# Optimization experiments

Measured on AMD Instinct MI355X. Metric: run time of the kernel, lower is better.

## Reference

```python
import jax, jax.numpy as jnp
import numpy as np

EPS = 1e-12  # torch F.normalize default eps


def setup_inputs() -> dict:
    key = jax.random.key(0)
    ks = jax.random.split(key, 7)
    dim, heads = 128, 8
    b, c, s, h, w = 2, dim, 3, 128, 128
    sc = 1.0 / np.sqrt(dim)
    return {
        "x": jax.random.normal(ks[0], (b, c, s, h, w), dtype=jnp.float32),
        "Wq": jax.random.normal(ks[1], (dim, dim), dtype=jnp.float32) * sc,
        "Wk": jax.random.normal(ks[2], (dim, dim), dtype=jnp.float32) * sc,
        "Wv": jax.random.normal(ks[3], (dim, dim), dtype=jnp.float32) * sc,
        "Wp": jax.random.normal(ks[4], (dim, dim), dtype=jnp.float32) * sc,
        "bp": jax.random.normal(ks[5], (dim,), dtype=jnp.float32) * 0.01,
        "rescale": jnp.ones((heads, 1, 1), dtype=jnp.float32),
    }


def _l2norm(t):
    # torch F.normalize(p=2, dim=-1): t / max(||t||, eps)
    n = jnp.sqrt(jnp.sum(t * t, axis=-1, keepdims=True))
    return t / jnp.maximum(n, EPS)


def reference(x, Wq, Wk, Wv, Wp, bp, rescale):
    b, c, s, h, w = x.shape
    heads = rescale.shape[0]
    d = c // heads
    n = h * w * s
    # [b,c,s,h,w] -> [b,h,w,s,c] -> [b, n, c]
    xt = jnp.transpose(x, (0, 3, 4, 2, 1)).reshape(b, n, c)
    # torch Linear: y = x @ W.T
    q = xt @ Wq.T
    k = xt @ Wk.T
    v = xt @ Wv.T
    # [b,n,heads,d] -> [b,heads,d,n] (channel attention: tokens along last axis)
    def to_heads(t):
        return jnp.transpose(t.reshape(b, n, heads, d), (0, 2, 3, 1))
    q, k, v = to_heads(q), to_heads(k), to_heads(v)
    q = _l2norm(q)
    k = _l2norm(k)
    # attn: [b,heads,d,d] = k @ q^T over token axis n
    attn = jnp.einsum('bhdn,bhen->bhde', k, q)
    attn = attn * rescale  # rescale broadcasts as [heads,1,1]
    attn = jax.nn.softmax(attn, axis=-1)
    out = jnp.einsum('bhde,bhen->bhdn', attn, v)  # [b,heads,d,n]
    # [b,heads,d,n] -> [b,n,heads*d]
    out = jnp.transpose(out, (0, 3, 1, 2)).reshape(b, n, c)
    out = out @ Wp.T + bp
    # [b,n,c] -> [b,h,w,s,c] -> [b,h,w,c,s] -> [b,c,s,h,w]
    out = out.reshape(b, h, w, s, c)
    out = jnp.transpose(out, (0, 1, 2, 4, 3))
    out = jnp.transpose(out, (0, 3, 4, 1, 2))
    return out
```

## Files before the change

### kernel.cpp

```cpp
#include <hip/hip_runtime.h>
#include <hip/hip_bf16.h>

typedef __bf16 bf16_t;
typedef __bf16 bf16x4 __attribute__((ext_vector_type(4)));
typedef __bf16 bf16x8 __attribute__((ext_vector_type(8)));
typedef float f32x4 __attribute__((ext_vector_type(4)));

#define NTOK 49152
#define CDIM 128
#define CHUNKS 128
#define KT 384
#define STEPS 12

__device__ inline f32x4 mfma16(bf16x8 a, bf16x8 b, f32x4 c) {
  return __builtin_amdgcn_mfma_f32_16x16x32_bf16(a, b, c, 0, 0, 0);
}

#define BARRIER() do { asm volatile("s_waitcnt lgkmcnt(0)" ::: "memory"); \
    __builtin_amdgcn_s_barrier(); } while (0)

#define STAGE_LOAD(st, step)                               \
  {                                                        \
    const float* p_ = gsrc + (step) * 32;                  \
    st[0] = *(const f32x4*)(p_ + 0);                       \
    st[1] = *(const f32x4*)(p_ + 4);                       \
    st[2] = *(const f32x4*)(p_ + 8);                       \
    st[3] = *(const f32x4*)(p_ + 12);                      \
  }
#define CVT4(v) (bf16x4){(bf16_t)(v)[0], (bf16_t)(v)[1], (bf16_t)(v)[2], (bf16_t)(v)[3]}
#define STAGE_WRITE(st, buf)                               \
  {                                                        \
    bf16_t* t_ = &tile[buf][0];                            \
    *(bf16x4*)&t_[cg0 * 8 + 0] = CVT4(st[0]);              \
    *(bf16x4*)&t_[cg0 * 8 + 4] = CVT4(st[1]);              \
    *(bf16x4*)&t_[cg1 * 8 + 0] = CVT4(st[2]);              \
    *(bf16x4*)&t_[cg1 * 8 + 4] = CVT4(st[3]);              \
  }
#define MFMA_PHASE(buf)                                                     \
  {                                                                         \
    bf16x8 frag[8];                                                         \
    _Pragma("unroll")                                                       \
    for (int g = 0; g < 8; ++g)                                             \
      frag[g] = *(const bf16x8*)&tile[buf][(g * 64 + lane) * 8];            \
    bf16x8 a0, a1;                                                          \
    if (wave == 0)      { a0 = frag[0]; a1 = frag[1]; }                     \
    else if (wave == 1) { a0 = frag[2]; a1 = frag[3]; }                     \
    else if (wave == 2) { a0 = frag[4]; a1 = frag[5]; }                     \
    else                { a0 = frag[6]; a1 = frag[7]; }                     \
    _Pragma("unroll")                                                       \
    for (int j = 0; j < 8; ++j) {                                           \
      acc[0][j] = mfma16(a0, frag[j], acc[0][j]);                           \
      acc[1][j] = mfma16(a1, frag[j], acc[1][j]);                           \
    }                                                                       \
  }

__global__ __launch_bounds__(256) void k1_gram(const float* __restrict__ x,
                                               float* __restrict__ part) {
  const int blk = blockIdx.x;
  const int b = blk >> 7, chunk = blk & 127;
  const float* Xb = x + (size_t)b * CDIM * NTOK;
  const int tid = threadIdx.x, wave = tid >> 6, lane = tid & 63;

  __shared__ __align__(16) bf16_t tile[2][128 * 32];

  const int sch = tid >> 1, shalf = tid & 1;
  const float* gsrc = Xb + (size_t)sch * NTOK + chunk * KT + shalf * 16;
  const int c16base = ((sch >> 4) << 6) + (sch & 15);
  const int cg0 = c16base + ((shalf * 2) << 4);
  const int cg1 = c16base + ((shalf * 2 + 1) << 4);

  f32x4 stA[4], stB[4];
  f32x4 acc[2][8];
#pragma unroll
  for (int t = 0; t < 2; ++t)
#pragma unroll
    for (int j = 0; j < 8; ++j) acc[t][j] = (f32x4){0.f, 0.f, 0.f, 0.f};

  STAGE_LOAD(stA, 0);
  STAGE_WRITE(stA, 0);
  STAGE_LOAD(stB, 1);
  BARRIER();

  for (int kk = 0; kk < STEPS; kk += 2) {
    if (kk + 2 < STEPS) STAGE_LOAD(stA, kk + 2);
    STAGE_WRITE(stB, 1);
    MFMA_PHASE(0);
    BARRIER();
    if (kk + 3 < STEPS) STAGE_LOAD(stB, kk + 3);
    if (kk + 2 < STEPS) STAGE_WRITE(stA, 0);
    MFMA_PHASE(1);
    BARRIER();
  }

  float* pb = part + ((size_t)(b * CHUNKS + chunk) << 14);
#pragma unroll
  for (int t = 0; t < 2; ++t)
#pragma unroll
    for (int j = 0; j < 8; ++j)
      *(f32x4*)&pb[((((t * 8 + j) << 8) + tid) << 2)] = acc[t][j];
}

__global__ __launch_bounds__(256) void k2a_reduce(const float* __restrict__ part,
                                                  float* __restrict__ part2,
                                                  int* __restrict__ cntM) {
  const int gid = blockIdx.x * 256 + threadIdx.x;
  if (gid < 2) cntM[gid] = 0;
  const int e4 = gid & 4095, sl = (gid >> 12) & 7, b = gid >> 15;
  const float* p = part + ((size_t)(b * CHUNKS + sl * 16) << 14) + e4 * 4;
  f32x4 s = (f32x4){0.f, 0.f, 0.f, 0.f};
#pragma unroll 8
  for (int i = 0; i < 16; ++i) s += *(const f32x4*)(p + ((size_t)i << 14));
  *(f32x4*)(part2 + ((size_t)(b * 8 + sl) << 14) + e4 * 4) = s;
}

__global__ __launch_bounds__(256) void kmid(const float* __restrict__ part2,
                                            const float* __restrict__ Wk,
                                            const float* __restrict__ Wq,
                                            const float* __restrict__ Wp,
                                            const float* __restrict__ Wv,
                                            const float* __restrict__ resc,
                                            float* __restrict__ Mbuf,
                                            bf16_t* __restrict__ Phi,
                                            int* __restrict__ cntM) {
  const int blk = blockIdx.x;
  const int b = blk >> 3, h = blk & 7;
  const int tid = threadIdx.x;

  __shared__ float S_l[128][132];
  __shared__ float Wk_l[16][128], Wq_l[16][128];
  __shared__ float Tk_l[16][132], Tq_l[16][132];
  __shared__ float A_l[16][16];
  __shared__ float dK[16], dQ[16];

  {
    const float* p0 = part2 + ((size_t)(b * 8) << 14);
#pragma unroll 1
    for (int k = 0; k < 16; ++k) {
      const int g4 = k * 256 + tid;
      f32x4 s = (f32x4){0.f, 0.f, 0.f, 0.f};
#pragma unroll
      for (int sl = 0; sl < 8; ++sl)
        s += *(const f32x4*)(p0 + ((size_t)sl << 14) + g4 * 4);
      const int tj = g4 >> 8, t_ = tj >> 3, j_ = tj & 7;
      const int t2 = g4 & 255, w2 = t2 >> 6, q2 = (t2 >> 4) & 3, r2 = t2 & 15;
      const int row0 = w2 * 32 + t_ * 16 + q2 * 4, col = j_ * 16 + r2;
#pragma unroll
      for (int reg = 0; reg < 4; ++reg) S_l[row0 + reg][col] = s[reg];
    }
#pragma unroll
    for (int k = 0; k < 8; ++k) {
      const int idx = k * 256 + tid;
      Wk_l[idx >> 7][idx & 127] = Wk[h * 2048 + idx];
      Wq_l[idx >> 7][idx & 127] = Wq[h * 2048 + idx];
    }
  }
  __syncthreads();

  {
    const int d2 = tid >> 5;
    const int j0 = (tid & 31) * 4;
    f32x4 aK0 = (f32x4){0.f,0.f,0.f,0.f}, aK1 = (f32x4){0.f,0.f,0.f,0.f};
    f32x4 aQ0 = (f32x4){0.f,0.f,0.f,0.f}, aQ1 = (f32x4){0.f,0.f,0.f,0.f};
#pragma unroll 1
    for (int cb = 0; cb < 4; ++cb) {
      f32x4 wk0[8], wk1[8], wq0[8], wq1[8];
#pragma unroll
      for (int q = 0; q < 8; ++q) {
        wk0[q] = *(const f32x4*)&Wk_l[d2][cb * 32 + q * 4];
        wk1[q] = *(const f32x4*)&Wk_l[d2 + 8][cb * 32 + q * 4];
        wq0[q] = *(const f32x4*)&Wq_l[d2][cb * 32 + q * 4];
        wq1[q] = *(const f32x4*)&Wq_l[d2 + 8][cb * 32 + q * 4];
      }
#pragma unroll
      for (int q = 0; q < 8; ++q) {
#pragma unroll
        for (int cc = 0; cc < 4; ++cc) {
          const int c = cb * 32 + q * 4 + cc;
          const f32x4 sv = *(const f32x4*)&S_l[c][j0];
          aK0 += sv * wk0[q][cc];
          aK1 += sv * wk1[q][cc];
          aQ0 += sv * wq0[q][cc];
          aQ1 += sv * wq1[q][cc];
        }
      }
    }
    *(f32x4*)&Tk_l[d2][j0]     = aK0;
    *(f32x4*)&Tk_l[d2 + 8][j0] = aK1;
    *(f32x4*)&Tq_l[d2][j0]     = aQ0;
    *(f32x4*)&Tq_l[d2 + 8][j0] = aQ1;
  }
  __syncthreads();

  {
    const int d = tid >> 4, e = tid & 15;
    f32x4 gacc = (f32x4){0.f,0.f,0.f,0.f};
    f32x4 kacc = (f32x4){0.f,0.f,0.f,0.f};
    f32x4 qacc = (f32x4){0.f,0.f,0.f,0.f};
#pragma unroll
    for (int j4 = 0; j4 < 32; ++j4) {
      const f32x4 tk = *(const f32x4*)&Tk_l[d][j4 * 4];
      const f32x4 wq = *(const f32x4*)&Wq_l[e][j4 * 4];
      gacc += tk * wq;
      if (e == 0) kacc += tk * (*(const f32x4*)&Wk_l[d][j4 * 4]);
      if (d == 0) qacc += (*(const f32x4*)&Tq_l[e][j4 * 4]) * wq;
    }
    if (e == 0) dK[d] = kacc[0] + kacc[1] + kacc[2] + kacc[3];
    if (d == 0) dQ[e] = qacc[0] + qacc[1] + qacc[2] + qacc[3];
    __syncthreads();
    const float g = gacc[0] + gacc[1] + gacc[2] + gacc[3];
    const float nk = fmaxf(sqrtf(fmaxf(dK[d], 0.f)), 1e-12f);
    const float nq = fmaxf(sqrtf(fmaxf(dQ[e], 0.f)), 1e-12f);
    float pre = g / (nk * nq) * resc[h];
    float mx = pre;
#pragma unroll
    for (int m = 1; m < 16; m <<= 1) mx = fmaxf(mx, __shfl_xor(mx, m, 64));
    const float p = expf(pre - mx);
    float sum = p;
#pragma unroll
    for (int m = 1; m < 16; m <<= 1) sum += __shfl_xor(sum, m, 64);
    A_l[d][e] = p / sum;
  }
  __syncthreads();

  {
    const int e = tid & 15, rg = tid >> 4;
#pragma unroll
    for (int k = 0; k < 8; ++k) {
      const int r = rg * 8 + k;
      const f32x4* wp4 = (const f32x4*)(Wp + r * 128 + h * 16);
      float m = 0.f;
#pragma unroll
      for (int q = 0; q < 4; ++q) {
        const f32x4 w = wp4[q];
        m += w[0] * A_l[q * 4 + 0][e] + w[1] * A_l[q * 4 + 1][e] +
             w[2] * A_l[q * 4 + 2][e] + w[3] * A_l[q * 4 + 3][e];
      }
      Mbuf[(size_t)b * 16384 + r * 128 + h * 16 + e] = m;
    }
  }

  __threadfence();
  __syncthreads();
  if (tid == 0) {
    atomicAdd(&cntM[b], 1);
    while (__hip_atomic_load(&cntM[b], __ATOMIC_RELAXED,
                             __HIP_MEMORY_SCOPE_AGENT) < 8)
      __builtin_amdgcn_s_sleep(16);
  }
  __syncthreads();
  __threadfence();

  {
    const int cc = tid & 15, rg = tid >> 4;
    const float* Mb = Mbuf + (size_t)b * 16384;
    float pacc[8] = {0.f, 0.f, 0.f, 0.f, 0.f, 0.f, 0.f, 0.f};
#pragma unroll 2
    for (int j4 = 0; j4 < 32; ++j4) {
      float wv[4];
#pragma unroll
      for (int jj = 0; jj < 4; ++jj)
        wv[jj] = Wv[(j4 * 4 + jj) * 128 + h * 16 + cc];
#pragma unroll
      for (int k = 0; k < 8; ++k) {
        const f32x4 m4 = *(const f32x4*)&Mb[(rg * 8 + k) * 128 + j4 * 4];
        pacc[k] += m4[0] * wv[0] + m4[1] * wv[1] + m4[2] * wv[2] + m4[3] * wv[3];
      }
    }
#pragma unroll
    for (int k = 0; k < 8; ++k)
      Phi[((size_t)b << 14) + (rg * 8 + k) * 128 + h * 16 + cc] = (bf16_t)pacc[k];
  }
}

__global__ __launch_bounds__(256) void k4_out(const float* __restrict__ x,
                                              const bf16_t* __restrict__ Phi,
                                              const float* __restrict__ bp,
                                              float* __restrict__ out) {
  const int blk = blockIdx.x;
  const int b = blk / 768, tg = blk % 768;
  const float* Xb = x + (size_t)b * CDIM * NTOK;
  const bf16_t* Ph = Phi + ((size_t)b << 14);
  float* Ob = out + (size_t)b * CDIM * NTOK;
  const int tid = threadIdx.x, wave = tid >> 6, lane = tid & 63;
  const int r = lane & 15, quad = lane >> 4;
  const int tok0 = tg * 64;

  __shared__ __align__(16) char smem[64 * 68 * 4];
  bf16_t* tile = (bf16_t*)smem;
  float* tbuf = (float*)smem;

  {
    const int sch = tid >> 1, shalf = tid & 1;
    const float* p = Xb + (size_t)sch * NTOK + tok0 + shalf * 32;
    f32x4 st[8];
#pragma unroll
    for (int q = 0; q < 8; ++q) st[q] = *(const f32x4*)(p + q * 4);
    const int chunk_hi = ((sch >> 5) << 8) + (((sch >> 3) & 3) << 4);
    const int ei = sch & 7;
#pragma unroll
    for (int j = 0; j < 32; ++j) {
      const int tok = shalf * 32 + j;
      const int chunk = chunk_hi + ((tok >> 4) << 6) + (tok & 15);
      tile[chunk * 8 + ei] = (bf16_t)st[j >> 2][j & 3];
    }
  }
  __syncthreads();

  f32x4 acc[8];
#pragma unroll
  for (int m = 0; m < 8; ++m) acc[m] = (f32x4){0.f, 0.f, 0.f, 0.f};

#pragma unroll
  for (int step = 0; step < 4; ++step) {
    const bf16x8 bfr = *(const bf16x8*)&tile[(step * 256 + wave * 64 + lane) * 8];
#pragma unroll
    for (int m = 0; m < 8; ++m) {
      const bf16x8 ah = *(const bf16x8*)(Ph + (16 * m + r) * 128 + step * 32 + quad * 8);
      acc[m] = mfma16(ah, bfr, acc[m]);
    }
  }

  __syncthreads();
#pragma unroll
  for (int half = 0; half < 2; ++half) {
#pragma unroll
    for (int mm = 0; mm < 4; ++mm) {
#pragma unroll
      for (int reg = 0; reg < 4; ++reg)
        tbuf[(mm * 16 + quad * 4 + reg) * 68 + wave * 16 + r] = acc[half * 4 + mm][reg];
    }
    __syncthreads();
#pragma unroll
    for (int rep = 0; rep < 4; ++rep) {
      const int idx = rep * 256 + tid, rloc = idx >> 4, g = idx & 15;
      f32x4 v = *(const f32x4*)&tbuf[rloc * 68 + g * 4];
      const int row = half * 64 + rloc;
      const float bb = bp[row];
      v[0] += bb; v[1] += bb; v[2] += bb; v[3] += bb;
      *(f32x4*)&Ob[(size_t)row * NTOK + tok0 + g * 4] = v;
    }
    if (half == 0) __syncthreads();
  }
}

extern "C" void kernel_launch(void* const* d_in, const int* in_sizes, int n_in,
                              void* d_out, int out_size, void* d_ws, size_t ws_size,
                              hipStream_t stream) {
  const float* x    = (const float*)d_in[0];
  const float* Wq   = (const float*)d_in[1];
  const float* Wk   = (const float*)d_in[2];
  const float* Wv   = (const float*)d_in[3];
  const float* Wp   = (const float*)d_in[4];
  const float* bp   = (const float*)d_in[5];
  const float* resc = (const float*)d_in[6];
  float* out = (float*)d_out;

  char* ws = (char*)d_ws;
  float*  Mbuf = (float*)(ws + 0);
  bf16_t* Phi  = (bf16_t*)(ws + 131072);
  int*    cntM = (int*)(ws + 196608);
  float* part  = (float*)d_out;
  float* part2 = (float*)((char*)d_out + 16777216);

  k1_gram<<<2 * CHUNKS, 256, 0, stream>>>(x, part);
  k2a_reduce<<<256, 256, 0, stream>>>(part, part2, cntM);
  kmid<<<16, 256, 0, stream>>>(part2, Wk, Wq, Wp, Wv, resc, Mbuf, Phi, cntM);
  k4_out<<<1536, 256, 0, stream>>>(x, Phi, bp, out);
}
```

Before: 184.9 us.

## Split mid-stage: single-pass Gram reduce, separate attn kernel and parallel Phi kernel

The two-level partial reduction (16-way then 8-way) becomes a single 128-way reduction kernel that writes the de-permuted S matrix directly. The middle kernel now only computes the softmax attention. A new 256-block kernel then builds Phi = Wp·A·Wv, replacing the 16-block kernel that used an atomic spin-wait barrier. The aim is to spread the small matrix work over more blocks and remove the inter-block spin. In exchange it adds one launch, and k2s uses scalar strided loads over 128 partials with only 128 blocks.

Result: faster. 178.6 us (-3.4%).

```diff
diff --git a/kernel.cpp b/kernel.cpp
--- a/kernel.cpp
+++ b/kernel.cpp
@@ -100,28 +100,32 @@
       *(f32x4*)&pb[((((t * 8 + j) << 8) + tid) << 2)] = acc[t][j];
 }
 
-__global__ __launch_bounds__(256) void k2a_reduce(const float* __restrict__ part,
-                                                  float* __restrict__ part2,
-                                                  int* __restrict__ cntM) {
+__global__ __launch_bounds__(256) void k2s(const float* __restrict__ part,
+                                           float* __restrict__ S) {
   const int gid = blockIdx.x * 256 + threadIdx.x;
-  if (gid < 2) cntM[gid] = 0;
-  const int e4 = gid & 4095, sl = (gid >> 12) & 7, b = gid >> 15;
-  const float* p = part + ((size_t)(b * CHUNKS + sl * 16) << 14) + e4 * 4;
-  f32x4 s = (f32x4){0.f, 0.f, 0.f, 0.f};
+  const int e = gid & 16383, b = gid >> 14;
+  const float* p = part + ((size_t)b << 21) + e;
+  float a0 = 0.f, a1 = 0.f, a2 = 0.f, a3 = 0.f;
 #pragma unroll 8
-  for (int i = 0; i < 16; ++i) s += *(const f32x4*)(p + ((size_t)i << 14));
-  *(f32x4*)(part2 + ((size_t)(b * 8 + sl) << 14) + e4 * 4) = s;
-}
-
-__global__ __launch_bounds__(256) void kmid(const float* __restrict__ part2,
-                                            const float* __restrict__ Wk,
-                                            const float* __restrict__ Wq,
-                                            const float* __restrict__ Wp,
-                                            const float* __restrict__ Wv,
-                                            const float* __restrict__ resc,
-                                            float* __restrict__ Mbuf,
-                                            bf16_t* __restrict__ Phi,
-                                            int* __restrict__ cntM) {
+  for (int i = 0; i < 128; i += 4) {
+    a0 += p[(size_t)(i + 0) << 14];
+    a1 += p[(size_t)(i + 1) << 14];
+    a2 += p[(size_t)(i + 2) << 14];
+    a3 += p[(size_t)(i + 3) << 14];
+  }
+  const float s = (a0 + a1) + (a2 + a3);
+  const int g4 = e >> 2, rg = e & 3;
+  const int tj = g4 >> 8, t = tj >> 3, j = tj & 7;
+  const int t2 = g4 & 255, w2 = t2 >> 6, q2 = (t2 >> 4) & 3, r2 = t2 & 15;
+  const int row = w2 * 32 + t * 16 + q2 * 4 + rg, col = j * 16 + r2;
+  S[((size_t)b << 14) + row * 128 + col] = s;
+}
+
+__global__ __launch_bounds__(256) void kattn(const float* __restrict__ S,
+                                             const float* __restrict__ Wk,
+                                             const float* __restrict__ Wq,
+                                             const float* __restrict__ resc,
+                                             float* __restrict__ attn) {
   const int blk = blockIdx.x;
   const int b = blk >> 3, h = blk & 7;
   const int tid = threadIdx.x;
@@ -129,23 +133,15 @@
   __shared__ float S_l[128][132];
   __shared__ float Wk_l[16][128], Wq_l[16][128];
   __shared__ float Tk_l[16][132], Tq_l[16][132];
-  __shared__ float A_l[16][16];
   __shared__ float dK[16], dQ[16];
 
   {
-    const float* p0 = part2 + ((size_t)(b * 8) << 14);
-#pragma unroll 1
-    for (int k = 0; k < 16; ++k) {
-      const int g4 = k * 256 + tid;
-      f32x4 s = (f32x4){0.f, 0.f, 0.f, 0.f};
-#pragma unroll
-      for (int sl = 0; sl < 8; ++sl)
-        s += *(const f32x4*)(p0 + ((size_t)sl << 14) + g4 * 4);
-      const int tj = g4 >> 8, t_ = tj >> 3, j_ = tj & 7;
-      const int t2 = g4 & 255, w2 = t2 >> 6, q2 = (t2 >> 4) & 3, r2 = t2 & 15;
-      const int row0 = w2 * 32 + t_ * 16 + q2 * 4, col = j_ * 16 + r2;
-#pragma unroll
-      for (int reg = 0; reg < 4; ++reg) S_l[row0 + reg][col] = s[reg];
+    const float* Sb = S + ((size_t)b << 14);
+#pragma unroll
+    for (int q = 0; q < 16; ++q) {
+      const int idx = q * 256 + tid;
+      const int row = idx >> 5, c4 = (idx & 31) << 2;
+      *(f32x4*)&S_l[row][c4] = *(const f32x4*)(Sb + row * 128 + c4);
     }
 #pragma unroll
     for (int k = 0; k < 8; ++k) {
@@ -218,57 +214,34 @@
     float sum = p;
 #pragma unroll
     for (int m = 1; m < 16; m <<= 1) sum += __shfl_xor(sum, m, 64);
-    A_l[d][e] = p / sum;
-  }
-  __syncthreads();
-
-  {
-    const int e = tid & 15, rg = tid >> 4;
-#pragma unroll
-    for (int k = 0; k < 8; ++k) {
-      const int r = rg * 8 + k;
-      const f32x4* wp4 = (const f32x4*)(Wp + r * 128 + h * 16);
-      float m = 0.f;
-#pragma unroll
-      for (int q = 0; q < 4; ++q) {
-        const f32x4 w = wp4[q];
-        m += w[0] * A_l[q * 4 + 0][e] + w[1] * A_l[q * 4 + 1][e] +
-             w[2] * A_l[q * 4 + 2][e] + w[3] * A_l[q * 4 + 3][e];
-      }
-      Mbuf[(size_t)b * 16384 + r * 128 + h * 16 + e] = m;
-    }
-  }
-
-  __threadfence();
-  __syncthreads();
-  if (tid == 0) {
-    atomicAdd(&cntM[b], 1);
-    while (__hip_atomic_load(&cntM[b], __ATOMIC_RELAXED,
-                             __HIP_MEMORY_SCOPE_AGENT) < 8)
-      __builtin_amdgcn_s_sleep(16);
-  }
-  __syncthreads();
-  __threadfence();
-
-  {
-    const int cc = tid & 15, rg = tid >> 4;
-    const float* Mb = Mbuf + (size_t)b * 16384;
-    float pacc[8] = {0.f, 0.f, 0.f, 0.f, 0.f, 0.f, 0.f, 0.f};
-#pragma unroll 2
-    for (int j4 = 0; j4 < 32; ++j4) {
-      float wv[4];
-#pragma unroll
-      for (int jj = 0; jj < 4; ++jj)
-        wv[jj] = Wv[(j4 * 4 + jj) * 128 + h * 16 + cc];
-#pragma unroll
-      for (int k = 0; k < 8; ++k) {
-        const f32x4 m4 = *(const f32x4*)&Mb[(rg * 8 + k) * 128 + j4 * 4];
-        pacc[k] += m4[0] * wv[0] + m4[1] * wv[1] + m4[2] * wv[2] + m4[3] * wv[3];
-      }
-    }
-#pragma unroll
-    for (int k = 0; k < 8; ++k)
-      Phi[((size_t)b << 14) + (rg * 8 + k) * 128 + h * 16 + cc] = (bf16_t)pacc[k];
+    attn[blk * 256 + tid] = p / sum;
+  }
+}
+
+__global__ __launch_bounds__(256) void k3_p(const float* __restrict__ attn,
+                                            const float* __restrict__ Wp,
+                                            const float* __restrict__ Wv,
+                                            bf16_t* __restrict__ Phi) {
+  const int blk = blockIdx.x;
+  const int b = blk >> 7, rrow = blk & 127;
+  const int tid = threadIdx.x;
+  __shared__ float M[128];
+  if (tid < 128) {
+    const int h = tid >> 4, e = tid & 15;
+    const float* A = attn + (size_t)(b * 8 + h) * 256;
+    const float* wp = Wp + rrow * 128 + h * 16;
+    float m = 0.f;
+#pragma unroll
+    for (int d = 0; d < 16; ++d) m += wp[d] * A[d * 16 + e];
+    M[tid] = m;
+  }
+  __syncthreads();
+  if (tid < 128) {
+    const int c = tid;
+    float p = 0.f;
+#pragma unroll 4
+    for (int j = 0; j < 128; ++j) p += M[j] * Wv[j * 128 + c];
+    Phi[((size_t)b << 14) + rrow * 128 + c] = (bf16_t)p;
   }
 }
 
@@ -356,14 +329,14 @@
   float* out = (float*)d_out;
 
   char* ws = (char*)d_ws;
-  float*  Mbuf = (float*)(ws + 0);
-  bf16_t* Phi  = (bf16_t*)(ws + 131072);
-  int*    cntM = (int*)(ws + 196608);
+  float*  S    = (float*)(ws + 0);
+  float*  attn = (float*)(ws + 131072);
+  bf16_t* Phi  = (bf16_t*)(ws + 147456);
   float* part  = (float*)d_out;
-  float* part2 = (float*)((char*)d_out + 16777216);
 
   k1_gram<<<2 * CHUNKS, 256, 0, stream>>>(x, part);
-  k2a_reduce<<<256, 256, 0, stream>>>(part, part2, cntM);
-  kmid<<<16, 256, 0, stream>>>(part2, Wk, Wq, Wp, Wv, resc, Mbuf, Phi, cntM);
+  k2s<<<128, 256, 0, stream>>>(part, S);
+  kattn<<<16, 256, 0, stream>>>(S, Wk, Wq, resc, attn);
+  k3_p<<<256, 256, 0, stream>>>(attn, Wp, Wv, Phi);
   k4_out<<<1536, 256, 0, stream>>>(x, Phi, bp, out);
 }
```
